# Performance work log

Hardware: AMD Instinct MI355X
Metric: run time of the kernel (lower is better)

Reference implementation:

```python
import jax, jax.numpy as jnp
import numpy as np

N_NODES, NUM_GRAPHS, MAX_N = 65536, 512, 192
D, H = 512, 8
DH = D // H


def setup_inputs() -> dict:
    key = jax.random.key(0)
    ks = jax.random.split(key, 13)
    s = 1.0 / np.sqrt(D).astype(np.float32)
    return {
        "node_features": jax.random.normal(ks[0], (N_NODES, D), jnp.float32),
        "batch_indices": jnp.sort(jax.random.randint(ks[1], (N_NODES,), 0, NUM_GRAPHS)),
        "global_query": jax.random.normal(ks[2], (1, H, 1, DH), jnp.float32) * s,
        "w_q": jax.random.normal(ks[3], (D, D), jnp.float32) * s,
        "b_q": jax.random.normal(ks[4], (D,), jnp.float32) * 0.02,
        "w_k": jax.random.normal(ks[5], (D, D), jnp.float32) * s,
        "b_k": jax.random.normal(ks[6], (D,), jnp.float32) * 0.02,
        "w_v": jax.random.normal(ks[7], (D, D), jnp.float32) * s,
        "b_v": jax.random.normal(ks[8], (D,), jnp.float32) * 0.02,
        "w_o": jax.random.normal(ks[9], (D, D), jnp.float32) * s,
        "b_o": jax.random.normal(ks[10], (D,), jnp.float32) * 0.02,
        "w_p": jax.random.normal(ks[11], (D, D), jnp.float32) * s,
        "b_p": jax.random.normal(ks[12], (D,), jnp.float32) * 0.02,
    }


def reference(node_features, batch_indices, global_query, w_q, b_q, w_k, b_k,
              w_v, b_v, w_o, b_o, w_p, b_p):
    # ragged bookkeeping (batch_indices is sorted)
    counts = jax.ops.segment_sum(jnp.ones_like(batch_indices), batch_indices,
                                 num_segments=NUM_GRAPHS)            # [G]
    offsets = jnp.cumsum(counts) - counts                            # [G]
    pos = jnp.arange(N_NODES) - offsets[batch_indices]               # local node pos

    # pad nodes to dense [G, MAX_N, D]
    dense = jnp.zeros((NUM_GRAPHS, MAX_N, D), node_features.dtype)
    dense = dense.at[batch_indices, pos].set(node_features)
    mask = jnp.zeros((NUM_GRAPHS, MAX_N), bool).at[batch_indices, pos].set(True)

    # Faithful replication of torch's expand+reshape of global_query:
    # Q_in[g, t, d] = gq_flat[h*DH + d%DH] with h = (t*D + d) // (n_g*DH)
    gqf = global_query.reshape(H * DH)
    t = jnp.arange(MAX_N)[:, None]                                   # [MAX_N,1]
    d = jnp.arange(D)[None, :]                                       # [1,D]
    n = jnp.maximum(counts, 1)[:, None, None]                        # [G,1,1]
    h = jnp.clip((t * D + d)[None] // (n * DH), 0, H - 1)            # [G,MAX_N,D]
    q_in = gqf[h * DH + (d % DH)[None]]                              # [G,MAX_N,D]

    Q = (q_in @ w_q.T + b_q).reshape(NUM_GRAPHS, MAX_N, H, DH)
    K = (dense @ w_k.T + b_k).reshape(NUM_GRAPHS, MAX_N, H, DH)
    V = (dense @ w_v.T + b_v).reshape(NUM_GRAPHS, MAX_N, H, DH)

    scale = 1.0 / np.sqrt(DH).astype(np.float32)
    scores = jnp.einsum('gthd,gshd->ghts', Q, K) * scale             # [G,H,T,S]
    scores = jnp.where(mask[:, None, None, :], scores, -1e9)
    attn_w = jax.nn.softmax(scores, axis=-1)
    attn = jnp.einsum('ghts,gshd->gthd', attn_w, V).reshape(NUM_GRAPHS, MAX_N, D)
    attn = attn @ w_o.T + b_o

    denom = jnp.maximum(counts, 1).astype(attn.dtype)[:, None]
    pooled = (attn * mask[..., None].astype(attn.dtype)).sum(axis=1) / denom
    return jax.nn.relu(pooled @ w_p.T + b_p)                         # [G, D]
```

## Files before the change

### kernel.cpp

```cpp
#include <hip/hip_runtime.h>
#include <hip/hip_bf16.h>
#include <cstdint>

typedef __bf16 bf16;
typedef __attribute__((ext_vector_type(8))) __bf16 bf16x8;
typedef __attribute__((ext_vector_type(4))) __bf16 bf16x4;
typedef __attribute__((ext_vector_type(2))) __bf16 bf16x2;
typedef __attribute__((ext_vector_type(4))) float f32x4;

#define N_NODES    65536
#define NUM_GRAPHS 512
#define MAX_N      192
#define D          512
#define H          8
#define DH         64
#define UMAX       64
#define USTRIDE    132

__device__ __forceinline__ void gload_lds16(const void* g, void* l) {
    __builtin_amdgcn_global_load_lds((const __attribute__((address_space(1))) void*)g,
                                     (__attribute__((address_space(3))) void*)l, 16, 0, 0);
}

__global__ __launch_bounds__(256) void lb_kernel(const int* __restrict__ batch,
                                                 int* __restrict__ lb) {
    int g = blockIdx.x * 256 + threadIdx.x;
    if (g > NUM_GRAPHS) return;
    int lo = 0, hi = N_NODES;
    while (lo < hi) {
        int mid = (lo + hi) >> 1;
        if (batch[mid] < g) lo = mid + 1; else hi = mid;
    }
    lb[g] = lo;
}

__global__ __launch_bounds__(192) void dedup_kernel(const int* __restrict__ lb,
                                                    int* __restrict__ udata) {
    const int g = blockIdx.x;
    const int off = lb[g];
    const int n = min(lb[g + 1] - off, MAX_N);
    __shared__ int keys[MAX_N];
    const int t = threadIdx.x;
    if (t < n) {
        unsigned un = (unsigned)n;
        int key = 0;
        #pragma unroll
        for (int p = 0; p < 8; p++) key |= (int)(((unsigned)(8 * t + p)) / un) << (3 * p);
        keys[t] = key;
    }
    __syncthreads();
    if (t == 0) {
        int* base = udata + (size_t)g * USTRIDE;
        int nu = 0;
        for (int s = 0; s < n; s++) {
            if (s == 0 || keys[s] != keys[s - 1]) {
                if (nu < UMAX) { base[1 + nu] = keys[s]; base[65 + nu] = 0; nu++; }
            }
            base[65 + (nu - 1)] += 1;
        }
        base[0] = nu;
    }
}

__global__ __launch_bounds__(256) void cvt_kernel(const float* __restrict__ src,
                                                  bf16* __restrict__ dst, int n) {
    int i = (blockIdx.x * 256 + threadIdx.x) * 4;
    if (i >= n) return;
    float4 v = *(const float4*)(src + i);
    bf16x4 o = {(bf16)v.x, (bf16)v.y, (bf16)v.z, (bf16)v.w};
    *(bf16x4*)(dst + i) = o;
}

__global__ __launch_bounds__(256) void p2_kernel(const float* __restrict__ gq,
                                                 const float* __restrict__ wq,
                                                 float* __restrict__ P2) {
    int h = blockIdx.x, p = blockIdx.y;
    __shared__ float gs[64];
    if (threadIdx.x < 64) gs[threadIdx.x] = gq[h * 64 + threadIdx.x];
    __syncthreads();
    for (int o = threadIdx.x; o < D; o += 256) {
        const float* wr = wq + (size_t)o * D + p * 64;
        float acc = 0.f;
        #pragma unroll 16
        for (int j = 0; j < 64; j++) acc += gs[j] * wr[j];
        P2[(size_t)(h * 8 + p) * D + o] = acc;
    }
}

__global__ __launch_bounds__(256) void wov_kernel(const float* __restrict__ wo,
                                                  const float* __restrict__ wv,
                                                  bf16* __restrict__ Wov) {
    const int ot = blockIdx.x;
    const int h  = blockIdx.y;
    __shared__ float wos[32 * 64];
    for (int idx = threadIdx.x; idx < 32 * 64; idx += 256) {
        int ol = idx >> 6, j = idx & 63;
        wos[idx] = wo[(size_t)(ot * 32 + ol) * D + h * 64 + j];
    }
    __syncthreads();
    const int c = threadIdx.x * 2;
    float acc0[32] = {}, acc1[32] = {};
    for (int j = 0; j < 64; j++) {
        float2 v2 = *(const float2*)(wv + (size_t)(h * 64 + j) * D + c);
        #pragma unroll
        for (int o = 0; o < 32; o++) {
            float wj = wos[o * 64 + j];
            acc0[o] += wj * v2.x; acc1[o] += wj * v2.y;
        }
    }
    #pragma unroll
    for (int o = 0; o < 32; o++) {
        bf16x2 r = {(bf16)acc0[o], (bf16)acc1[o]};
        *(bf16x2*)(Wov + (size_t)(ot * 32 + o) * 4096 + h * 512 + c) = r;
    }
}

__global__ __launch_bounds__(256) void cst_kernel(const float* __restrict__ wo,
                                                  const float* __restrict__ bv,
                                                  const float* __restrict__ bo,
                                                  float* __restrict__ cst) {
    int o = blockIdx.x * 256 + threadIdx.x;
    if (o >= D) return;
    const float* wr = wo + (size_t)o * D;
    float acc = bo[o];
    for (int d0 = 0; d0 < D; d0 += 4) {
        float4 wv4 = *(const float4*)(wr + d0);
        float4 b4  = *(const float4*)(bv + d0);
        acc += wv4.x * b4.x + wv4.y * b4.y + wv4.z * b4.z + wv4.w * b4.w;
    }
    cst[o] = acc;
}

__global__ __launch_bounds__(256) void k_gemm(const float* __restrict__ Af,
                                              const bf16* __restrict__ Wkb,
                                              const float* __restrict__ bkb,
                                              bf16* __restrict__ Kout) {
    const int lin = blockIdx.x;
    const int xcd = lin & 7;
    const int idx = lin >> 3;
    const int nt  = idx & 3;
    const int ml  = idx >> 2;
    const int i0 = (xcd * 64 + ml) * 128;
    const int o0 = nt * 128;

    __shared__ char smem[18432];
    bf16* As = (bf16*)smem;
    bf16* Bs = (bf16*)(smem + 10240);
    const int tid = threadIdx.x;
    const int lane = tid & 63;
    const int w = tid >> 6;
    const int wm = w & 1, wn = w >> 1;
    const int fr = lane & 15, quad = lane >> 4;
    const int sr = lane >> 2;
    const int sc = (lane & 3) * 8;
    const float* gA = Af + (size_t)(i0 + w * 32 + sr) * D + sc;
    const bf16*  gB = Wkb + (size_t)(o0 + w * 32 + sr) * D + sc;
    bf16* lA = As + (w * 32 + sr) * 40 + sc;
    bf16* lB = Bs + (w * 32) * 32;

    f32x4 acc[4][4] = {};

    for (int kt = 0; kt < D; kt += 32) {
        float4 a0 = *(const float4*)(gA + kt);
        float4 a1 = *(const float4*)(gA + kt + 4);
        float4 a2 = *(const float4*)(gA + (size_t)16 * D + kt);
        float4 a3 = *(const float4*)(gA + (size_t)16 * D + kt + 4);
        __syncthreads();
        gload_lds16(gB + kt, lB);
        gload_lds16(gB + (size_t)16 * D + kt, lB + 16 * 32);
        bf16x8 wA0 = {(bf16)a0.x,(bf16)a0.y,(bf16)a0.z,(bf16)a0.w,
                      (bf16)a1.x,(bf16)a1.y,(bf16)a1.z,(bf16)a1.w};
        bf16x8 wA1 = {(bf16)a2.x,(bf16)a2.y,(bf16)a2.z,(bf16)a2.w,
                      (bf16)a3.x,(bf16)a3.y,(bf16)a3.z,(bf16)a3.w};
        *(bf16x8*)lA = wA0;
        *(bf16x8*)(lA + 16 * 40) = wA1;
        __syncthreads();
        bf16x8 fa[4], fb[4];
        #pragma unroll
        for (int mf = 0; mf < 4; mf++)
            fa[mf] = *(const bf16x8*)(As + (wm * 64 + mf * 16 + fr) * 40 + quad * 8);
        #pragma unroll
        for (int nf = 0; nf < 4; nf++)
            fb[nf] = *(const bf16x8*)(Bs + (wn * 64 + nf * 16 + fr) * 32 + quad * 8);
        #pragma unroll
        for (int mf = 0; mf < 4; mf++)
            #pragma unroll
            for (int nf = 0; nf < 4; nf++)
                acc[mf][nf] = __builtin_amdgcn_mfma_f32_16x16x32_bf16(fa[mf], fb[nf], acc[mf][nf], 0, 0, 0);
    }

    bf16* Cs = (bf16*)smem;
    #pragma unroll
    for (int pass = 0; pass < 2; pass++) {
        __syncthreads();
        if (wm == pass) {
            #pragma unroll
            for (int nf = 0; nf < 4; nf++) {
                const int col = wn * 64 + nf * 16 + fr;
                const float bs = bkb[o0 + col];
                #pragma unroll
                for (int mf = 0; mf < 4; mf++) {
                    #pragma unroll
                    for (int r = 0; r < 4; r++)
                        Cs[(mf * 16 + quad * 4 + r) * 132 + col] = (bf16)(acc[mf][nf][r] + bs);
                }
            }
        }
        __syncthreads();
        #pragma unroll
        for (int k = 0; k < 4; k++) {
            int idx2 = k * 256 + tid;
            int row = idx2 >> 4;
            int coff = (idx2 & 15) * 8;
            bf16x8 v = *(const bf16x8*)(Cs + row * 132 + coff);
            *(bf16x8*)(Kout + (size_t)(i0 + pass * 64 + row) * D + o0 + coff) = v;
        }
    }
}

__global__ __launch_bounds__(512) void attn_kernel(const bf16* __restrict__ Kb,
                                                   const float* __restrict__ P2,
                                                   const float* __restrict__ bq,
                                                   const int* __restrict__ lb,
                                                   const int* __restrict__ udata,
                                                   const float* __restrict__ Af,
                                                   bf16* __restrict__ abar) {
    const int g = blockIdx.x;
    const int tid = threadIdx.x;
    const int lane = tid & 63;
    const int w = tid >> 6;
    const int h = w;
    const int off = lb[g];
    const int n = min(lb[g + 1] - off, MAX_N);

    __shared__ bf16 Qs[8][16 * 80];
    __shared__ float wacc[8][MAX_N];
    __shared__ int upat_l[UMAX], ucnt_l[UMAX];

    bf16* outg = abar + (size_t)g * 4096;
    if (n == 0) {
        const bf16 z0 = (bf16)0.f;
        bf16x8 z = {z0, z0, z0, z0, z0, z0, z0, z0};
        *(bf16x8*)(outg + tid * 8) = z;
        return;
    }

    const int* ubase = udata + (size_t)g * USTRIDE;
    const int nu = ubase[0];
    if (tid < 64) {
        upat_l[tid] = (tid < nu) ? ubase[1 + tid] : 0;
        ucnt_l[tid] = (tid < nu) ? ubase[65 + tid] : 0;
    }
    wacc[w][lane] = 0.f; wacc[w][64 + lane] = 0.f; wacc[w][128 + lane] = 0.f;
    __syncthreads();

    const int fr = lane & 15;
    const int quad = lane >> 4;
    const float inv_n = 1.0f / (float)n;

    for (int c0 = 0; c0 < nu; c0 += 16) {
        {
            const int ul = lane >> 2;
            const int j0 = (lane & 3) * 16;
            const bool valid = (c0 + ul) < nu;
            const int pat = upat_l[c0 + ul];
            const float* bpq = bq + h * 64 + j0;
            float4 q0 = *(const float4*)bpq;
            float4 q1 = *(const float4*)(bpq + 4);
            float4 q2 = *(const float4*)(bpq + 8);
            float4 q3 = *(const float4*)(bpq + 12);
            #pragma unroll
            for (int p = 0; p < 8; p++) {
                const int hp = (pat >> (3 * p)) & 7;
                const float* pp = P2 + (size_t)(hp * 8 + p) * D + h * 64 + j0;
                float4 t0 = *(const float4*)pp;
                float4 t1 = *(const float4*)(pp + 4);
                float4 t2 = *(const float4*)(pp + 8);
                float4 t3 = *(const float4*)(pp + 12);
                q0.x += t0.x; q0.y += t0.y; q0.z += t0.z; q0.w += t0.w;
                q1.x += t1.x; q1.y += t1.y; q1.z += t1.z; q1.w += t1.w;
                q2.x += t2.x; q2.y += t2.y; q2.z += t2.z; q2.w += t2.w;
                q3.x += t3.x; q3.y += t3.y; q3.z += t3.z; q3.w += t3.w;
            }
            if (!valid) {
                q0.x=q0.y=q0.z=q0.w=0.f; q1.x=q1.y=q1.z=q1.w=0.f;
                q2.x=q2.y=q2.z=q2.w=0.f; q3.x=q3.y=q3.z=q3.w=0.f;
            }
            bf16x8 b0 = {(bf16)q0.x,(bf16)q0.y,(bf16)q0.z,(bf16)q0.w,
                         (bf16)q1.x,(bf16)q1.y,(bf16)q1.z,(bf16)q1.w};
            bf16x8 b1 = {(bf16)q2.x,(bf16)q2.y,(bf16)q2.z,(bf16)q2.w,
                         (bf16)q3.x,(bf16)q3.y,(bf16)q3.z,(bf16)q3.w};
            *(bf16x8*)(&Qs[w][ul * 80 + j0])     = b0;
            *(bf16x8*)(&Qs[w][ul * 80 + j0 + 8]) = b1;
        }
        bf16x8 fa0 = *(const bf16x8*)(&Qs[w][fr * 80 + quad * 8]);
        bf16x8 fa1 = *(const bf16x8*)(&Qs[w][fr * 80 + 32 + quad * 8]);

        f32x4 sc[12];
        #pragma unroll
        for (int st = 0; st < 12; st++) {
            if (st * 16 < n) {
                int s = st * 16 + fr;
                int row = off + (s < n ? s : n - 1);
                const bf16* kp = Kb + (size_t)row * D + h * 64 + quad * 8;
                bf16x8 fb0 = *(const bf16x8*)kp;
                bf16x8 fb1 = *(const bf16x8*)(kp + 32);
                f32x4 a = {0.f, 0.f, 0.f, 0.f};
                a = __builtin_amdgcn_mfma_f32_16x16x32_bf16(fa0, fb0, a, 0, 0, 0);
                a = __builtin_amdgcn_mfma_f32_16x16x32_bf16(fa1, fb1, a, 0, 0, 0);
                if (s < n) {
                    sc[st].x = a.x * 0.125f; sc[st].y = a.y * 0.125f;
                    sc[st].z = a.z * 0.125f; sc[st].w = a.w * 0.125f;
                } else {
                    sc[st].x = sc[st].y = sc[st].z = sc[st].w = -1e30f;
                }
            } else {
                sc[st].x = sc[st].y = sc[st].z = sc[st].w = -1e30f;
            }
        }
        float m[4] = {-1e30f, -1e30f, -1e30f, -1e30f};
        #pragma unroll
        for (int st = 0; st < 12; st++) {
            m[0] = fmaxf(m[0], sc[st].x); m[1] = fmaxf(m[1], sc[st].y);
            m[2] = fmaxf(m[2], sc[st].z); m[3] = fmaxf(m[3], sc[st].w);
        }
        #pragma unroll
        for (int o = 1; o <= 8; o <<= 1) {
            #pragma unroll
            for (int r = 0; r < 4; r++) m[r] = fmaxf(m[r], __shfl_xor(m[r], o));
        }
        float den[4] = {0.f, 0.f, 0.f, 0.f};
        #pragma unroll
        for (int st = 0; st < 12; st++) {
            float e0 = __expf(sc[st].x - m[0]); float e1 = __expf(sc[st].y - m[1]);
            float e2 = __expf(sc[st].z - m[2]); float e3 = __expf(sc[st].w - m[3]);
            sc[st].x = e0; sc[st].y = e1; sc[st].z = e2; sc[st].w = e3;
            den[0] += e0; den[1] += e1; den[2] += e2; den[3] += e3;
        }
        #pragma unroll
        for (int o = 1; o <= 8; o <<= 1) {
            #pragma unroll
            for (int r = 0; r < 4; r++) den[r] += __shfl_xor(den[r], o);
        }
        float wf[4];
        #pragma unroll
        for (int r = 0; r < 4; r++)
            wf[r] = (float)ucnt_l[c0 + quad * 4 + r] * inv_n / den[r];
        #pragma unroll
        for (int st = 0; st < 12; st++) {
            float v = sc[st].x * wf[0] + sc[st].y * wf[1] + sc[st].z * wf[2] + sc[st].w * wf[3];
            v += __shfl_xor(v, 16);
            v += __shfl_xor(v, 32);
            if (lane < 16) wacc[w][st * 16 + lane] += v;
        }
    }

    __syncthreads();
    const int cp = lane * 8;
    const float* Ag = Af + (size_t)off * D + cp;
    const float* wp_ = wacc[w];
    float acc0[8] = {};
    for (int s = 0; s < n; s++) {
        float4 x0 = *(const float4*)(Ag + (size_t)s * D);
        float4 x1 = *(const float4*)(Ag + (size_t)s * D + 4);
        float wv = wp_[s];
        acc0[0] += wv * x0.x; acc0[1] += wv * x0.y;
        acc0[2] += wv * x0.z; acc0[3] += wv * x0.w;
        acc0[4] += wv * x1.x; acc0[5] += wv * x1.y;
        acc0[6] += wv * x1.z; acc0[7] += wv * x1.w;
    }
    bf16x8 r = {(bf16)acc0[0],(bf16)acc0[1],(bf16)acc0[2],(bf16)acc0[3],
                (bf16)acc0[4],(bf16)acc0[5],(bf16)acc0[6],(bf16)acc0[7]};
    *(bf16x8*)(outg + h * 512 + cp) = r;
}

__global__ __launch_bounds__(256) void zero_kernel(float* __restrict__ p, int n4) {
    int i = blockIdx.x * 256 + threadIdx.x;
    if (i < n4) { float4 z = {0.f, 0.f, 0.f, 0.f}; *(float4*)(p + i * 4) = z; }
}

__global__ __launch_bounds__(256) void og_gemm(const bf16* __restrict__ Ab,
                                               const bf16* __restrict__ Bb,
                                               float* __restrict__ Yt) {
    const int o0 = blockIdx.x * 128;
    const int i0 = blockIdx.y * 128;
    const int k0 = blockIdx.z * 512;
    __shared__ bf16 As[128 * 32];
    __shared__ bf16 Bs[128 * 32];
    const int tid = threadIdx.x;
    const int lane = tid & 63;
    const int w = tid >> 6;
    const int wm = w & 1, wn = w >> 1;
    const int fr = lane & 15, quad = lane >> 4;
    const bf16* gA = Ab + (size_t)(i0 + w * 32 + (lane >> 2)) * 4096 + k0 + (lane & 3) * 8;
    const bf16* gB = Bb + (size_t)(o0 + w * 32 + (lane >> 2)) * 4096 + k0 + (lane & 3) * 8;
    bf16* lA = As + (w * 32) * 32;
    bf16* lB = Bs + (w * 32) * 32;

    f32x4 acc[4][4] = {};

    for (int kt = 0; kt < 512; kt += 32) {
        __syncthreads();
        gload_lds16(gA + kt, lA);
        gload_lds16(gA + (size_t)16 * 4096 + kt, lA + 16 * 32);
        gload_lds16(gB + kt, lB);
        gload_lds16(gB + (size_t)16 * 4096 + kt, lB + 16 * 32);
        __syncthreads();
        bf16x8 fa[4], fb[4];
        #pragma unroll
        for (int mf = 0; mf < 4; mf++)
            fa[mf] = *(const bf16x8*)(As + (wm * 64 + mf * 16 + fr) * 32 + quad * 8);
        #pragma unroll
        for (int nf = 0; nf < 4; nf++)
            fb[nf] = *(const bf16x8*)(Bs + (wn * 64 + nf * 16 + fr) * 32 + quad * 8);
        #pragma unroll
        for (int mf = 0; mf < 4; mf++)
            #pragma unroll
            for (int nf = 0; nf < 4; nf++)
                acc[mf][nf] = __builtin_amdgcn_mfma_f32_16x16x32_bf16(fa[mf], fb[nf], acc[mf][nf], 0, 0, 0);
    }
    #pragma unroll
    for (int nf = 0; nf < 4; nf++) {
        const int col = o0 + wn * 64 + nf * 16 + fr;
        #pragma unroll
        for (int mf = 0; mf < 4; mf++) {
            const int row = i0 + wm * 64 + mf * 16 + quad * 4;
            #pragma unroll
            for (int r = 0; r < 4; r++)
                atomicAdd(&Yt[(size_t)(row + r) * D + col], acc[mf][nf][r]);
        }
    }
}

__global__ __launch_bounds__(256) void proj_p(const float* __restrict__ tmp,
                                              const float* __restrict__ cst,
                                              const bf16* __restrict__ Wpb,
                                              const float* __restrict__ bp,
                                              const int* __restrict__ lb,
                                              float* __restrict__ out) {
    const int o0 = blockIdx.x * 128;
    const int i0 = blockIdx.y * 128;
    __shared__ bf16 As[128 * 32];
    __shared__ bf16 Bs[128 * 32];
    const int tid = threadIdx.x;
    const int lane = tid & 63;
    const int w = tid >> 6;
    const int wm = w & 1, wn = w >> 1;
    const int fr = lane & 15, quad = lane >> 4;
    const int ar = tid >> 1;
    const int ac = (tid & 1) * 16;
    const int g = i0 + ar;
    const bool live = lb[g + 1] - lb[g] > 0;
    const float* tp = tmp + (size_t)g * D + ac;
    const float* cp = cst + ac;
    const bf16* gB = Wpb + (size_t)(o0 + w * 32 + (lane >> 2)) * D + (lane & 3) * 8;
    bf16* lB = Bs + (w * 32) * 32;

    f32x4 acc[4][4] = {};

    for (int kt = 0; kt < D; kt += 32) {
        __syncthreads();
        gload_lds16(gB + kt, lB);
        gload_lds16(gB + (size_t)16 * D + kt, lB + 16 * 32);
        {
            float4 x0 = *(const float4*)(tp + kt);
            float4 x1 = *(const float4*)(tp + kt + 4);
            float4 x2 = *(const float4*)(tp + kt + 8);
            float4 x3 = *(const float4*)(tp + kt + 12);
            float4 c0 = *(const float4*)(cp + kt);
            float4 c1 = *(const float4*)(cp + kt + 4);
            float4 c2 = *(const float4*)(cp + kt + 8);
            float4 c3 = *(const float4*)(cp + kt + 12);
            float s = live ? 1.f : 0.f;
            bf16x8 v0 = {(bf16)((x0.x+c0.x)*s),(bf16)((x0.y+c0.y)*s),(bf16)((x0.z+c0.z)*s),(bf16)((x0.w+c0.w)*s),
                         (bf16)((x1.x+c1.x)*s),(bf16)((x1.y+c1.y)*s),(bf16)((x1.z+c1.z)*s),(bf16)((x1.w+c1.w)*s)};
            bf16x8 v1 = {(bf16)((x2.x+c2.x)*s),(bf16)((x2.y+c2.y)*s),(bf16)((x2.z+c2.z)*s),(bf16)((x2.w+c2.w)*s),
                         (bf16)((x3.x+c3.x)*s),(bf16)((x3.y+c3.y)*s),(bf16)((x3.z+c3.z)*s),(bf16)((x3.w+c3.w)*s)};
            *(bf16x8*)(As + ar * 32 + ac) = v0;
            *(bf16x8*)(As + ar * 32 + ac + 8) = v1;
        }
        __syncthreads();
        bf16x8 fa[4], fb[4];
        #pragma unroll
        for (int mf = 0; mf < 4; mf++)
            fa[mf] = *(const bf16x8*)(As + (wm * 64 + mf * 16 + fr) * 32 + quad * 8);
        #pragma unroll
        for (int nf = 0; nf < 4; nf++)
            fb[nf] = *(const bf16x8*)(Bs + (wn * 64 + nf * 16 + fr) * 32 + quad * 8);
        #pragma unroll
        for (int mf = 0; mf < 4; mf++)
            #pragma unroll
            for (int nf = 0; nf < 4; nf++)
                acc[mf][nf] = __builtin_amdgcn_mfma_f32_16x16x32_bf16(fa[mf], fb[nf], acc[mf][nf], 0, 0, 0);
    }
    #pragma unroll
    for (int nf = 0; nf < 4; nf++) {
        const int col = o0 + wn * 64 + nf * 16 + fr;
        const float bs = bp[col];
        #pragma unroll
        for (int mf = 0; mf < 4; mf++) {
            const int row = i0 + wm * 64 + mf * 16 + quad * 4;
            #pragma unroll
            for (int r = 0; r < 4; r++)
                out[(size_t)(row + r) * D + col] = fmaxf(acc[mf][nf][r] + bs, 0.f);
        }
    }
}

extern "C" void kernel_launch(void* const* d_in, const int* in_sizes, int n_in,
                              void* d_out, int out_size, void* d_ws, size_t ws_size,
                              hipStream_t stream) {
    const float* nf    = (const float*)d_in[0];
    const int*   batch = (const int*)d_in[1];
    const float* gq    = (const float*)d_in[2];
    const float* wq    = (const float*)d_in[3];
    const float* bq    = (const float*)d_in[4];
    const float* wk    = (const float*)d_in[5];
    const float* bk    = (const float*)d_in[6];
    const float* wv    = (const float*)d_in[7];
    const float* bv    = (const float*)d_in[8];
    const float* wo    = (const float*)d_in[9];
    const float* bo    = (const float*)d_in[10];
    const float* wp    = (const float*)d_in[11];
    const float* bp    = (const float*)d_in[12];
    float* out = (float*)d_out;

    char* ws = (char*)d_ws;
    bf16*  abar = (bf16*)(ws + ((size_t)2 << 20));
    bf16*  Wov  = (bf16*)(ws + ((size_t)6 << 20));
    float* tmp  = (float*)(ws + ((size_t)10 << 20));
    float* cst  = (float*)(ws + ((size_t)11 << 20));
    bf16*  Kb   = (bf16*)(ws + ((size_t)64 << 20));
    char* sm = ws + ((size_t)128 << 20);
    int*  lb    = (int*)sm;    sm += 4096;
    int*  udata = (int*)sm;    sm += (size_t)NUM_GRAPHS * USTRIDE * 4 + 2048;
    bf16* Wkb   = (bf16*)sm;   sm += (size_t)D * D * 2;
    bf16* Wpb   = (bf16*)sm;   sm += (size_t)D * D * 2;
    float* P2   = (float*)sm;  sm += (size_t)64 * D * 4;

    lb_kernel<<<3, 256, 0, stream>>>(batch, lb);
    dedup_kernel<<<NUM_GRAPHS, 192, 0, stream>>>(lb, udata);
    cvt_kernel<<<(D * D / 4) / 256, 256, 0, stream>>>(wk, Wkb, D * D);
    cvt_kernel<<<(D * D / 4) / 256, 256, 0, stream>>>(wp, Wpb, D * D);
    p2_kernel<<<dim3(8, 8), 256, 0, stream>>>(gq, wq, P2);
    k_gemm<<<2048, 256, 0, stream>>>(nf, Wkb, bk, Kb);
    wov_kernel<<<dim3(16, 8), 256, 0, stream>>>(wo, wv, Wov);
    cst_kernel<<<2, 256, 0, stream>>>(wo, bv, bo, cst);
    attn_kernel<<<NUM_GRAPHS, 512, 0, stream>>>(Kb, P2, bq, lb, udata, nf, abar);
    zero_kernel<<<(NUM_GRAPHS * D / 4 + 255) / 256, 256, 0, stream>>>(tmp, NUM_GRAPHS * D / 4);
    og_gemm<<<dim3(4, 4, 8), 256, 0, stream>>>(abar, Wov, tmp);
    proj_p<<<dim3(4, 4), 256, 0, stream>>>(tmp, cst, Wpb, bp, lb, out);
}
```

Baseline: 451.1 us.

## Register-prefetch next K tile in k_gemm and restructure pooled weighted-sum loop

The K-projection GEMM now loads the next k-tile of A (fp32) and B (bf16) into registers while MFMAs run on the current tile. B is staged through registers with padded LDS rows instead of using async global-to-LDS loads, which overlaps global latency with compute and reduces bank conflicts. Separately, the final pooling loop in the attention kernel has each thread handle one feature column for all heads, so each node row is read once rather than once per head. The cost is higher register pressure and larger shared memory in the GEMM.

```diff
diff --git a/kernel.cpp b/kernel.cpp
--- a/kernel.cpp
+++ b/kernel.cpp
@@ -143,7 +143,7 @@
     const int i0 = (xcd * 64 + ml) * 128;
     const int o0 = nt * 128;
 
-    __shared__ char smem[18432];
+    __shared__ char smem[20480];
     bf16* As = (bf16*)smem;
     bf16* Bs = (bf16*)(smem + 10240);
     const int tid = threadIdx.x;
@@ -156,24 +156,27 @@
     const float* gA = Af + (size_t)(i0 + w * 32 + sr) * D + sc;
     const bf16*  gB = Wkb + (size_t)(o0 + w * 32 + sr) * D + sc;
     bf16* lA = As + (w * 32 + sr) * 40 + sc;
-    bf16* lB = Bs + (w * 32) * 32;
+    bf16* lB = Bs + (w * 32 + sr) * 40 + sc;
 
     f32x4 acc[4][4] = {};
 
+    float4 a0 = *(const float4*)(gA);
+    float4 a1 = *(const float4*)(gA + 4);
+    float4 a2 = *(const float4*)(gA + (size_t)16 * D);
+    float4 a3 = *(const float4*)(gA + (size_t)16 * D + 4);
+    bf16x8 pb0 = *(const bf16x8*)(gB);
+    bf16x8 pb1 = *(const bf16x8*)(gB + (size_t)16 * D);
+
     for (int kt = 0; kt < D; kt += 32) {
-        float4 a0 = *(const float4*)(gA + kt);
-        float4 a1 = *(const float4*)(gA + kt + 4);
-        float4 a2 = *(const float4*)(gA + (size_t)16 * D + kt);
-        float4 a3 = *(const float4*)(gA + (size_t)16 * D + kt + 4);
-        __syncthreads();
-        gload_lds16(gB + kt, lB);
-        gload_lds16(gB + (size_t)16 * D + kt, lB + 16 * 32);
+        __syncthreads();
         bf16x8 wA0 = {(bf16)a0.x,(bf16)a0.y,(bf16)a0.z,(bf16)a0.w,
                       (bf16)a1.x,(bf16)a1.y,(bf16)a1.z,(bf16)a1.w};
         bf16x8 wA1 = {(bf16)a2.x,(bf16)a2.y,(bf16)a2.z,(bf16)a2.w,
                       (bf16)a3.x,(bf16)a3.y,(bf16)a3.z,(bf16)a3.w};
         *(bf16x8*)lA = wA0;
         *(bf16x8*)(lA + 16 * 40) = wA1;
+        *(bf16x8*)lB = pb0;
+        *(bf16x8*)(lB + 16 * 40) = pb1;
         __syncthreads();
         bf16x8 fa[4], fb[4];
         #pragma unroll
@@ -181,7 +184,15 @@
             fa[mf] = *(const bf16x8*)(As + (wm * 64 + mf * 16 + fr) * 40 + quad * 8);
         #pragma unroll
         for (int nf = 0; nf < 4; nf++)
-            fb[nf] = *(const bf16x8*)(Bs + (wn * 64 + nf * 16 + fr) * 32 + quad * 8);
+            fb[nf] = *(const bf16x8*)(Bs + (wn * 64 + nf * 16 + fr) * 40 + quad * 8);
+        if (kt + 32 < D) {
+            a0 = *(const float4*)(gA + kt + 32);
+            a1 = *(const float4*)(gA + kt + 36);
+            a2 = *(const float4*)(gA + (size_t)16 * D + kt + 32);
+            a3 = *(const float4*)(gA + (size_t)16 * D + kt + 36);
+            pb0 = *(const bf16x8*)(gB + kt + 32);
+            pb1 = *(const bf16x8*)(gB + (size_t)16 * D + kt + 32);
+        }
         #pragma unroll
         for (int mf = 0; mf < 4; mf++)
             #pragma unroll
@@ -356,22 +367,15 @@
     }
 
     __syncthreads();
-    const int cp = lane * 8;
-    const float* Ag = Af + (size_t)off * D + cp;
-    const float* wp_ = wacc[w];
-    float acc0[8] = {};
+    const float* Ac = Af + (size_t)off * D + tid;
+    float accv[8] = {};
     for (int s = 0; s < n; s++) {
-        float4 x0 = *(const float4*)(Ag + (size_t)s * D);
-        float4 x1 = *(const float4*)(Ag + (size_t)s * D + 4);
-        float wv = wp_[s];
-        acc0[0] += wv * x0.x; acc0[1] += wv * x0.y;
-        acc0[2] += wv * x0.z; acc0[3] += wv * x0.w;
-        acc0[4] += wv * x1.x; acc0[5] += wv * x1.y;
-        acc0[6] += wv * x1.z; acc0[7] += wv * x1.w;
-    }
-    bf16x8 r = {(bf16)acc0[0],(bf16)acc0[1],(bf16)acc0[2],(bf16)acc0[3],
-                (bf16)acc0[4],(bf16)acc0[5],(bf16)acc0[6],(bf16)acc0[7]};
-    *(bf16x8*)(outg + h * 512 + cp) = r;
+        float av = Ac[(size_t)s * D];
+        #pragma unroll
+        for (int hh = 0; hh < 8; hh++) accv[hh] += wacc[hh][s] * av;
+    }
+    #pragma unroll
+    for (int hh = 0; hh < 8; hh++) outg[hh * 512 + tid] = (bf16)accv[hh];
 }
 
 __global__ __launch_bounds__(256) void zero_kernel(float* __restrict__ p, int n4) {
```

Result: faster. 436.6 us (-3.2%).
